# Performance work log

Measured on AMD Instinct MI355X. Metric: run time of the kernel, lower is better.

The kernel has to match this reference:

```python
import jax, jax.numpy as jnp
import numpy as np

DK = 64  # head dim = n_features // n_heads = 512 // 8


def setup_inputs() -> dict:
    key = jax.random.key(0)
    ks = jax.random.split(key, 6)
    B, N, D = 2, 4096, 512
    feature = jax.random.normal(ks[0], (B, N, D), dtype=jnp.float32)
    Sh = jax.random.normal(ks[1], (B, N, N), dtype=jnp.float32)
    Sw = jax.random.normal(ks[2], (B, N, N), dtype=jnp.float32)
    # torch Linear weights are [out, in]; xavier-uniform init
    lim = np.sqrt(6.0 / (D + DK)).astype(np.float32)
    wq_w = jax.random.uniform(ks[3], (DK, D), jnp.float32, -lim, lim)
    wk_w = jax.random.uniform(ks[4], (DK, D), jnp.float32, -lim, lim)
    wv_w = jax.random.uniform(ks[5], (DK, D), jnp.float32, -lim, lim)
    zb = jnp.zeros((DK,), jnp.float32)
    return {"feature": feature, "Sh": Sh, "Sw": Sw,
            "wq_w": wq_w, "wq_b": zb, "wk_w": wk_w, "wk_b": zb,
            "wv_w": wv_w, "wv_b": zb}


def reference(feature, Sh, Sw, wq_w, wq_b, wk_w, wk_b, wv_w, wv_b):
    # Linear projections (torch: x @ W.T + b)
    Q = jnp.einsum('bnd,kd->bnk', feature, wq_w) + wq_b  # [B,N,dk]
    K = jnp.einsum('bnd,kd->bnk', feature, wk_w) + wk_b  # [B,N,dk]
    V = jnp.einsum('bnd,kd->bnk', feature, wv_w) + wv_b  # [B,N,dv]
    sqrt_dk = jnp.sqrt(jnp.float32(Q.shape[-1]))
    # scores = (QK^T + Sh + Sw) / sqrt(dk)  -- biases added BEFORE scaling,
    # exactly as in attnFunc
    A = (jnp.einsum('bqk,bnk->bqn', Q, K) + Sh + Sw) / sqrt_dk  # [B,N,N]
    A = jax.nn.softmax(A, axis=-1)
    return jnp.einsum('bqn,bnk->bqk', A, V)  # [B,N,dv]
```

## Files before the change

### kernel.cpp

```cpp
#include <hip/hip_runtime.h>
#include <hip/hip_bf16.h>


typedef short bf16x8 __attribute__((ext_vector_type(8)));
typedef short bf16x4 __attribute__((ext_vector_type(4)));
typedef float f32x4  __attribute__((ext_vector_type(4)));

#if __has_builtin(__builtin_amdgcn_exp2f)
#define EXP2F(x) __builtin_amdgcn_exp2f(x)
#else
#define EXP2F(x) exp2f(x)
#endif
#if __has_builtin(__builtin_amdgcn_rcpf)
#define RCPF(x) __builtin_amdgcn_rcpf(x)
#else
#define RCPF(x) (1.0f / (x))
#endif

__device__ __forceinline__ f32x4 mfma16(bf16x8 a, bf16x8 b, f32x4 c) {
  return __builtin_amdgcn_mfma_f32_16x16x32_bf16(a, b, c, 0, 0, 0);
}
__device__ __forceinline__ short f2b(float x) {
  __hip_bfloat16 h = __float2bfloat16(x);
  return __builtin_bit_cast(short, h);
}
__device__ __forceinline__ float b2f(short s) {
  return __bfloat162float(__builtin_bit_cast(__hip_bfloat16, s));
}
__device__ __forceinline__ void split_hl(float x, short& h, short& l) {
  __hip_bfloat16 bh = __float2bfloat16(x);
  h = __builtin_bit_cast(short, bh);
  l = f2b(x - __bfloat162float(bh));
}

__global__ void wcvt_kernel(const float* __restrict__ wq, const float* __restrict__ wk,
                            const float* __restrict__ wv,
                            short* __restrict__ wh, short* __restrict__ wl) {
  int idx = (blockIdx.x * 256 + threadIdx.x) * 4;
  int p = idx >> 15;
  int off = idx & 32767;
  const float* src = (p == 0) ? wq : (p == 1) ? wk : wv;
  f32x4 v = *(const f32x4*)(src + off);
  bf16x4 h, l;
#pragma unroll
  for (int j = 0; j < 4; ++j) { short hh, ll; split_hl(v[j], hh, ll); h[j] = hh; l[j] = ll; }
  *(bf16x4*)(wh + p * 32768 + off) = h;
  *(bf16x4*)(wl + p * 32768 + off) = l;
}

__global__ __launch_bounds__(256) void proj_kernel(
    const float* __restrict__ feat, const short* __restrict__ wh, const short* __restrict__ wl,
    const float* __restrict__ bq, const float* __restrict__ bk, const float* __restrict__ bv,
    short* __restrict__ Qh, short* __restrict__ Ql,
    short* __restrict__ Kh, short* __restrict__ Kl, short* __restrict__ Vt) {
  const int lane = threadIdx.x & 63, wave = threadIdx.x >> 6;
  const int lq = lane & 15, quad = lane >> 4;
  const int wid = blockIdx.x * 4 + wave;
  const int p = wid >> 9, rg = wid & 511;
  const int rbase = rg * 16;
  const float Cs = 0.18033688011112042f;

  f32x4 acc[4];
#pragma unroll
  for (int t = 0; t < 4; ++t) acc[t] = (f32x4){0.f, 0.f, 0.f, 0.f};

  const float* frow = feat + (size_t)(rbase + lq) * 512 + quad * 8;
  const int wrow = p * 64;
  for (int ks = 0; ks < 16; ++ks) {
    f32x4 f0 = *(const f32x4*)(frow + ks * 32);
    f32x4 f1 = *(const f32x4*)(frow + ks * 32 + 4);
    bf16x8 fh, fl;
#pragma unroll
    for (int j = 0; j < 4; ++j) {
      short hh, ll;
      split_hl(f0[j], hh, ll); fh[j] = hh; fl[j] = ll;
      split_hl(f1[j], hh, ll); fh[j + 4] = hh; fl[j + 4] = ll;
    }
#pragma unroll
    for (int t = 0; t < 4; ++t) {
      const int wo = (wrow + t * 16 + lq) * 512 + ks * 32 + quad * 8;
      bf16x8 wfh = *(const bf16x8*)(wh + wo);
      bf16x8 wfl = *(const bf16x8*)(wl + wo);
      acc[t] = mfma16(fh, wfh, acc[t]);
      acc[t] = mfma16(fl, wfh, acc[t]);
      acc[t] = mfma16(fh, wfl, acc[t]);
    }
  }
  const int b = rbase >> 12, rloc = rbase & 4095;
  if (p == 0) {
#pragma unroll
    for (int t = 0; t < 4; ++t) {
      const int dk = t * 16 + lq;
      const float bb = bq[dk];
#pragma unroll
      for (int r = 0; r < 4; ++r) {
        const int row = rbase + 4 * quad + r;
        short h, l;
        split_hl((acc[t][r] + bb) * Cs, h, l);
        Qh[row * 64 + dk] = h; Ql[row * 64 + dk] = l;
      }
    }
  } else if (p == 1) {
#pragma unroll
    for (int t = 0; t < 4; ++t) {
      const int dk = t * 16 + lq;
      const float bb = bk[dk];
#pragma unroll
      for (int r = 0; r < 4; ++r) {
        const int row = rbase + 4 * quad + r;
        short h, l;
        split_hl(acc[t][r] + bb, h, l);
        Kh[row * 64 + dk] = h; Kl[row * 64 + dk] = l;
      }
    }
  } else {
#pragma unroll
    for (int t = 0; t < 4; ++t) {
      const int dk = t * 16 + lq;
      const float bb = bv[dk];
      bf16x4 vpack;
#pragma unroll
      for (int r = 0; r < 4; ++r) vpack[r] = f2b(acc[t][r] + bb);
      *(bf16x4*)(Vt + (size_t)(b * 64 + dk) * 4096 + rloc + 4 * quad) = vpack;
    }
  }
}

__global__ __launch_bounds__(256, 4) void attn_kernel(
    const float* __restrict__ Sh, const float* __restrict__ Sw,
    const short* __restrict__ Qh, const short* __restrict__ Ql,
    const short* __restrict__ Kh, const short* __restrict__ Vt,
    float* __restrict__ Opart, float* __restrict__ lpart) {
  __shared__ short Plds[4][16][72];
  __shared__ short BiasLds[4][16][520];
  const int bid = blockIdx.x;
  const int sp = bid & 7, qt = (bid >> 3) & 63, b = bid >> 9;
  const int tid = threadIdx.x;
  const int wave = tid >> 6, lane = tid & 63, lq = lane & 15, quad = lane >> 4;
  const int qbase = qt * 64 + wave * 16;
  const float Cs = 0.18033688011112042f;

  const int qidx = (b * 4096 + qbase + lq) * 64 + quad * 8;
  const bf16x8 qfh0 = *(const bf16x8*)(Qh + qidx);
  const bf16x8 qfh1 = *(const bf16x8*)(Qh + qidx + 32);
  const bf16x8 qfl0 = *(const bf16x8*)(Ql + qidx);
  const bf16x8 qfl1 = *(const bf16x8*)(Ql + qidx + 32);

  short* bw = &BiasLds[wave][0][0];
  const float* shp = Sh + (size_t)(b * 4096 + qbase) * 4096 + sp * 512;
  const float* swp = Sw + (size_t)(b * 4096 + qbase) * 4096 + sp * 512;
  f32x4 sa[4], sc[4];
#pragma unroll
  for (int i = 0; i < 4; ++i) {
    const size_t off = (size_t)(i >> 1) * 4096 + (i & 1) * 256 + lane * 4;
    sa[i] = __builtin_nontemporal_load((const f32x4*)(shp + off));
    sc[i] = __builtin_nontemporal_load((const f32x4*)(swp + off));
  }
#pragma unroll 4
  for (int i = 0; i < 32; ++i) {
    const int sl = i & 3;
    f32x4 s = (sa[sl] + sc[sl]) * Cs;
    bf16x4 pk;
#pragma unroll
    for (int j = 0; j < 4; ++j) pk[j] = f2b(s[j]);
    *(bf16x4*)(bw + (i >> 1) * 520 + (i & 1) * 256 + lane * 4) = pk;
    if (i + 4 < 32) {
      const int in = i + 4;
      const size_t off = (size_t)(in >> 1) * 4096 + (in & 1) * 256 + lane * 4;
      sa[sl] = __builtin_nontemporal_load((const f32x4*)(shp + off));
      sc[sl] = __builtin_nontemporal_load((const f32x4*)(swp + off));
    }
  }

  f32x4 accO[4];
#pragma unroll
  for (int u = 0; u < 4; ++u) accO[u] = (f32x4){0.f, 0.f, 0.f, 0.f};
  float lsum = 0.f;
  short* pw = &Plds[wave][0][0];
  const short* vbase = Vt + (size_t)b * 64 * 4096;

  for (int it = 0; it < 8; ++it) {
    const int kb = sp * 512 + it * 64;
    bf16x8 kh0[4], kh1[4];
#pragma unroll
    for (int t = 0; t < 4; ++t) {
      const int kidx = (b * 4096 + kb + t * 16 + lq) * 64 + quad * 8;
      kh0[t] = *(const bf16x8*)(Kh + kidx);
      kh1[t] = *(const bf16x8*)(Kh + kidx + 32);
    }
    f32x4 accS[4];
#pragma unroll
    for (int t = 0; t < 4; ++t) accS[t] = (f32x4){0.f, 0.f, 0.f, 0.f};
#pragma unroll
    for (int t = 0; t < 4; ++t) {
      accS[t] = mfma16(kh0[t], qfh0, accS[t]);
      accS[t] = mfma16(kh1[t], qfh1, accS[t]);
      accS[t] = mfma16(kh0[t], qfl0, accS[t]);
      accS[t] = mfma16(kh1[t], qfl1, accS[t]);
    }
#pragma unroll
    for (int t = 0; t < 4; ++t) {
      const bf16x4 bb = *(const bf16x4*)(bw + lq * 520 + it * 64 + 16 * t + 4 * quad);
      bf16x4 pk;
#pragma unroll
      for (int r = 0; r < 4; ++r) {
        float s = accS[t][r] + b2f(bb[r]);
        float p = EXP2F(s);
        lsum += p;
        pk[r] = f2b(p);
      }
      *(bf16x4*)(pw + lq * 72 + 16 * t + 4 * quad) = pk;
    }
#pragma unroll
    for (int c = 0; c < 2; ++c) {
      const bf16x8 pa = *(const bf16x8*)(pw + lq * 72 + c * 32 + quad * 8);
#pragma unroll
      for (int u = 0; u < 4; ++u) {
        const bf16x8 vf = *(const bf16x8*)(vbase + (size_t)(u * 16 + lq) * 4096 + kb + c * 32 + quad * 8);
        accO[u] = mfma16(pa, vf, accO[u]);
      }
    }
  }
  lsum += __shfl_xor(lsum, 16, 64);
  lsum += __shfl_xor(lsum, 32, 64);

  const int orowW = sp * 8192 + b * 4096 + qbase;
  if (quad == 0) lpart[orowW + lq] = lsum;
#pragma unroll
  for (int u = 0; u < 4; ++u)
#pragma unroll
    for (int r = 0; r < 4; ++r)
      Opart[(size_t)(orowW + 4 * quad + r) * 64 + u * 16 + lq] = accO[u][r];
}

__global__ void combine_kernel(const float* __restrict__ Opart, const float* __restrict__ lpart,
                               float* __restrict__ out) {
  const int g = blockIdx.x * 256 + threadIdx.x;
  const int row = g >> 4;
  f32x4 o = (f32x4){0.f, 0.f, 0.f, 0.f};
  float l = 0.f;
#pragma unroll
  for (int s = 0; s < 8; ++s) {
    o += __builtin_nontemporal_load((const f32x4*)(Opart + (size_t)s * 524288 + g * 4));
    l += lpart[s * 8192 + row];
  }
  const float rl = RCPF(l);
  *(f32x4*)(out + g * 4) = o * rl;
}

extern "C" void kernel_launch(void* const* d_in, const int* in_sizes, int n_in,
                              void* d_out, int out_size, void* d_ws, size_t ws_size,
                              hipStream_t stream) {
  const float* feature = (const float*)d_in[0];
  const float* Sh = (const float*)d_in[1];
  const float* Sw = (const float*)d_in[2];
  const float* wq = (const float*)d_in[3];
  const float* bq = (const float*)d_in[4];
  const float* wk = (const float*)d_in[5];
  const float* bk = (const float*)d_in[6];
  const float* wv = (const float*)d_in[7];
  const float* bv = (const float*)d_in[8];

  char* ws = (char*)d_ws;
  const size_t MB = 1u << 20;
  short* Qh = (short*)(ws + 0 * MB);
  short* Ql = (short*)(ws + 1 * MB);
  short* Kh = (short*)(ws + 2 * MB);
  short* Kl = (short*)(ws + 3 * MB);
  short* Vt = (short*)(ws + 4 * MB);
  short* wh = (short*)(ws + 5 * MB);
  short* wl = (short*)(ws + 5 * MB + 262144);
  float* lpart = (float*)(ws + 5 * MB + 524288);
  float* Opart = (float*)(ws + 6 * MB);

  wcvt_kernel<<<96, 256, 0, stream>>>(wq, wk, wv, wh, wl);
  proj_kernel<<<384, 256, 0, stream>>>(feature, wh, wl, bq, bk, bv, Qh, Ql, Kh, Kl, Vt);
  attn_kernel<<<1024, 256, 0, stream>>>(Sh, Sw, Qh, Ql, Kh, Vt, Opart, lpart);
  combine_kernel<<<512, 256, 0, stream>>>(Opart, lpart, (float*)d_out);
}
```

Measured before the change: 372.5 us.

## Stream bias tiles through double-buffered LDS interleaved with attention loop

Replaces the upfront staging of the full 16x512 bias slab per wave into LDS with a per-iteration 32-column tile, double-buffered in a much smaller LDS footprint. The loads of the next Sh/Sw tile are issued while the current tile's QK and PV MFMAs run, and the V fragments are loaded early, behind sched barriers. The goal is to overlap the dominant Sh/Sw memory streaming with compute and to cut LDS use so more blocks fit per CU. The trade-off is twice as many loop iterations with smaller MFMA batches, and the bias loads now use narrower 128-byte row segments.

Result: faster. 351.5 us (-5.6%).

```diff
diff --git a/kernel.cpp b/kernel.cpp
--- a/kernel.cpp
+++ b/kernel.cpp
@@ -131,8 +131,8 @@
     const short* __restrict__ Qh, const short* __restrict__ Ql,
     const short* __restrict__ Kh, const short* __restrict__ Vt,
     float* __restrict__ Opart, float* __restrict__ lpart) {
-  __shared__ short Plds[4][16][72];
-  __shared__ short BiasLds[4][16][520];
+  __shared__ short Plds[4][16][40];
+  __shared__ short BiasLds[4][2][16][36];
   const int bid = blockIdx.x;
   const int sp = bid & 7, qt = (bid >> 3) & 63, b = bid >> 9;
   const int tid = threadIdx.x;
@@ -140,67 +140,85 @@
   const int qbase = qt * 64 + wave * 16;
   const float Cs = 0.18033688011112042f;
 
+  const float* shp = Sh + (size_t)(b * 4096 + qbase) * 4096 + sp * 512;
+  const float* swp = Sw + (size_t)(b * 4096 + qbase) * 4096 + sp * 512;
+  const int lrow = lane >> 3;
+  const int lcol = (lane & 7) * 4;
+
+  f32x4 sa[2], sc[2];
+#pragma unroll
+  for (int j = 0; j < 2; ++j) {
+    const size_t off = (size_t)(j * 8 + lrow) * 4096 + lcol;
+    sa[j] = __builtin_nontemporal_load((const f32x4*)(shp + off));
+    sc[j] = __builtin_nontemporal_load((const f32x4*)(swp + off));
+  }
+
   const int qidx = (b * 4096 + qbase + lq) * 64 + quad * 8;
   const bf16x8 qfh0 = *(const bf16x8*)(Qh + qidx);
   const bf16x8 qfh1 = *(const bf16x8*)(Qh + qidx + 32);
   const bf16x8 qfl0 = *(const bf16x8*)(Ql + qidx);
   const bf16x8 qfl1 = *(const bf16x8*)(Ql + qidx + 32);
 
-  short* bw = &BiasLds[wave][0][0];
-  const float* shp = Sh + (size_t)(b * 4096 + qbase) * 4096 + sp * 512;
-  const float* swp = Sw + (size_t)(b * 4096 + qbase) * 4096 + sp * 512;
-  f32x4 sa[4], sc[4];
-#pragma unroll
-  for (int i = 0; i < 4; ++i) {
-    const size_t off = (size_t)(i >> 1) * 4096 + (i & 1) * 256 + lane * 4;
-    sa[i] = __builtin_nontemporal_load((const f32x4*)(shp + off));
-    sc[i] = __builtin_nontemporal_load((const f32x4*)(swp + off));
-  }
-#pragma unroll 4
-  for (int i = 0; i < 32; ++i) {
-    const int sl = i & 3;
-    f32x4 s = (sa[sl] + sc[sl]) * Cs;
-    bf16x4 pk;
-#pragma unroll
-    for (int j = 0; j < 4; ++j) pk[j] = f2b(s[j]);
-    *(bf16x4*)(bw + (i >> 1) * 520 + (i & 1) * 256 + lane * 4) = pk;
-    if (i + 4 < 32) {
-      const int in = i + 4;
-      const size_t off = (size_t)(in >> 1) * 4096 + (in & 1) * 256 + lane * 4;
-      sa[sl] = __builtin_nontemporal_load((const f32x4*)(shp + off));
-      sc[sl] = __builtin_nontemporal_load((const f32x4*)(swp + off));
-    }
-  }
-
   f32x4 accO[4];
 #pragma unroll
   for (int u = 0; u < 4; ++u) accO[u] = (f32x4){0.f, 0.f, 0.f, 0.f};
   float lsum = 0.f;
   short* pw = &Plds[wave][0][0];
+  short* bw = &BiasLds[wave][0][0][0];
   const short* vbase = Vt + (size_t)b * 64 * 4096;
 
-  for (int it = 0; it < 8; ++it) {
-    const int kb = sp * 512 + it * 64;
-    bf16x8 kh0[4], kh1[4];
-#pragma unroll
-    for (int t = 0; t < 4; ++t) {
+#pragma unroll 2
+  for (int it = 0; it < 16; ++it) {
+    const int cur = it & 1;
+    short* bwc = bw + cur * 576;
+
+#pragma unroll
+    for (int j = 0; j < 2; ++j) {
+      f32x4 s = (sa[j] + sc[j]) * Cs;
+      bf16x4 pk;
+#pragma unroll
+      for (int r = 0; r < 4; ++r) pk[r] = f2b(s[r]);
+      *(bf16x4*)(bwc + (j * 8 + lrow) * 36 + lcol) = pk;
+    }
+
+    const int kb = sp * 512 + it * 32;
+    bf16x8 kh0[2], kh1[2];
+#pragma unroll
+    for (int t = 0; t < 2; ++t) {
       const int kidx = (b * 4096 + kb + t * 16 + lq) * 64 + quad * 8;
       kh0[t] = *(const bf16x8*)(Kh + kidx);
       kh1[t] = *(const bf16x8*)(Kh + kidx + 32);
     }
-    f32x4 accS[4];
-#pragma unroll
-    for (int t = 0; t < 4; ++t) accS[t] = (f32x4){0.f, 0.f, 0.f, 0.f};
-#pragma unroll
-    for (int t = 0; t < 4; ++t) {
+    bf16x8 vf[4];
+#pragma unroll
+    for (int u = 0; u < 4; ++u)
+      vf[u] = *(const bf16x8*)(vbase + (size_t)(u * 16 + lq) * 4096 + kb + quad * 8);
+    __builtin_amdgcn_sched_barrier(0);
+
+    if (it < 15) {
+#pragma unroll
+      for (int j = 0; j < 2; ++j) {
+        const size_t off = (size_t)(j * 8 + lrow) * 4096 + (it + 1) * 32 + lcol;
+        sa[j] = __builtin_nontemporal_load((const f32x4*)(shp + off));
+        sc[j] = __builtin_nontemporal_load((const f32x4*)(swp + off));
+      }
+    }
+    __builtin_amdgcn_sched_barrier(0);
+
+    f32x4 accS[2];
+#pragma unroll
+    for (int t = 0; t < 2; ++t) accS[t] = (f32x4){0.f, 0.f, 0.f, 0.f};
+#pragma unroll
+    for (int t = 0; t < 2; ++t) {
       accS[t] = mfma16(kh0[t], qfh0, accS[t]);
       accS[t] = mfma16(kh1[t], qfh1, accS[t]);
       accS[t] = mfma16(kh0[t], qfl0, accS[t]);
       accS[t] = mfma16(kh1[t], qfl1, accS[t]);
     }
-#pragma unroll
-    for (int t = 0; t < 4; ++t) {
-      const bf16x4 bb = *(const bf16x4*)(bw + lq * 520 + it * 64 + 16 * t + 4 * quad);
+
+#pragma unroll
+    for (int t = 0; t < 2; ++t) {
+      const bf16x4 bb = *(const bf16x4*)(bwc + lq * 36 + 16 * t + 4 * quad);
       bf16x4 pk;
 #pragma unroll
       for (int r = 0; r < 4; ++r) {
@@ -209,18 +227,14 @@
         lsum += p;
         pk[r] = f2b(p);
       }
-      *(bf16x4*)(pw + lq * 72 + 16 * t + 4 * quad) = pk;
-    }
-#pragma unroll
-    for (int c = 0; c < 2; ++c) {
-      const bf16x8 pa = *(const bf16x8*)(pw + lq * 72 + c * 32 + quad * 8);
-#pragma unroll
-      for (int u = 0; u < 4; ++u) {
-        const bf16x8 vf = *(const bf16x8*)(vbase + (size_t)(u * 16 + lq) * 4096 + kb + c * 32 + quad * 8);
-        accO[u] = mfma16(pa, vf, accO[u]);
-      }
-    }
-  }
+      *(bf16x4*)(pw + lq * 40 + 16 * t + 4 * quad) = pk;
+    }
+
+    const bf16x8 pa = *(const bf16x8*)(pw + lq * 40 + quad * 8);
+#pragma unroll
+    for (int u = 0; u < 4; ++u) accO[u] = mfma16(pa, vf[u], accO[u]);
+  }
+
   lsum += __shfl_xor(lsum, 16, 64);
   lsum += __shfl_xor(lsum, 32, 64);
 
```
